# Kernel tuning notes

Measured on AMD Instinct MI355X. Metric: run time of the kernel, lower is better.

Reference implementation:

```python
import jax, jax.numpy as jnp
import numpy as np

N, E, IN, HID, H, C = 10000, 320000, 64, 64, 4, 64
HC = H * C  # 256


def setup_inputs() -> dict:
    key = jax.random.key(0)
    ks = jax.random.split(key, 40)
    ki = iter(range(40))
    def nrm(shape, scale=0.05):
        return jax.random.normal(ks[next(ki)], shape, dtype=jnp.float32) * scale
    inp = {
        "x": jax.random.normal(ks[next(ki)], (N, IN), dtype=jnp.float32),
        "edge_index": jax.random.randint(ks[next(ki)], (2, E), 0, N, dtype=jnp.int64),
        "lin_w": nrm((IN, HID)), "lin_b": nrm((HID,)),
    }
    dims_in = [HID, HC, HC]
    for i, di in enumerate(dims_in):
        inp[f"gat_w{i}"] = nrm((di, HC))
        inp[f"att_src{i}"] = nrm((H, C))
        inp[f"att_dst{i}"] = nrm((H, C))
        inp[f"gat_b{i}"] = nrm((HC,))
        inp[f"ln_g{i}"] = jnp.ones((HC,), jnp.float32)
        inp[f"ln_b{i}"] = jnp.zeros((HC,), jnp.float32)
    inp["ffn_w1"] = nrm((HC, 2 * HID)); inp["ffn_b1"] = nrm((2 * HID,))
    inp["ffn_w2"] = nrm((2 * HID, 64)); inp["ffn_b2"] = nrm((64,))
    return inp


def _layernorm(x, g, b, eps=1e-5):
    m = jnp.mean(x, -1, keepdims=True)
    v = jnp.var(x, -1, keepdims=True)
    return (x - m) * jax.lax.rsqrt(v + eps) * g + b


def _gat(x, src, dst, w, a_src, a_dst, b):
    # PyG GATConv: per-head linear, additive attention, segment softmax over dst
    xl = (x @ w).reshape(-1, H, C)              # [N,H,C]
    e = jax.nn.leaky_relu(jnp.sum(xl * a_src, -1)[src]
                          + jnp.sum(xl * a_dst, -1)[dst], 0.2)  # [E,H]
    emax = jax.ops.segment_max(e, dst, num_segments=N)
    ex = jnp.exp(e - emax[dst])
    alpha = ex / jax.ops.segment_sum(ex, dst, num_segments=N)[dst]
    out = jax.ops.segment_sum(xl[src] * alpha[:, :, None], dst, num_segments=N)
    return out.reshape(-1, HC) + b


def reference(x, edge_index, lin_w, lin_b,
              gat_w0, att_src0, att_dst0, gat_b0, ln_g0, ln_b0,
              gat_w1, att_src1, att_dst1, gat_b1, ln_g1, ln_b1,
              gat_w2, att_src2, att_dst2, gat_b2, ln_g2, ln_b2,
              ffn_w1, ffn_b1, ffn_w2, ffn_b2):
    loops = jnp.arange(N, dtype=edge_index.dtype)
    src = jnp.concatenate([edge_index[0], loops])  # add_self_loops=True
    dst = jnp.concatenate([edge_index[1], loops])
    h = jax.nn.relu(x @ lin_w + lin_b)
    layers = [(gat_w0, att_src0, att_dst0, gat_b0, ln_g0, ln_b0),
              (gat_w1, att_src1, att_dst1, gat_b1, ln_g1, ln_b1),
              (gat_w2, att_src2, att_dst2, gat_b2, ln_g2, ln_b2)]
    for (w, a_s, a_d, b, g, lb) in layers:
        residual = h
        h = jax.nn.elu(_gat(h, src, dst, w, a_s, a_d, b))
        if residual.shape[-1] != h.shape[-1]:
            residual = jnp.pad(residual, ((0, 0), (0, h.shape[-1] - residual.shape[-1])))
        h = _layernorm(h + residual, g, lb)  # dropout is identity in eval mode
    h = jax.nn.relu(h @ ffn_w1 + ffn_b1)
    return h @ ffn_w2 + ffn_b2
```

## Files before the change

### kernel.cpp

```cpp
#include <hip/hip_runtime.h>

#define N_NODES 10000
#define N_EDGES 320000
#define EL (N_EDGES + N_NODES)
#define HC 256
#define CAP 96

using bf16x8 = __attribute__((ext_vector_type(8))) short;
using f32x4  = __attribute__((ext_vector_type(4))) float;

__device__ __forceinline__ float bf2f(unsigned short u) {
  union { unsigned int i; float f; } v; v.i = ((unsigned int)u) << 16; return v.f;
}
__device__ __forceinline__ unsigned short f2bf(float f) {
  union { float f; unsigned int i; } v; v.f = f;
  unsigned int r = (v.i + 0x7FFFu + ((v.i >> 16) & 1u)) >> 16;
  return (unsigned short)r;
}


__device__ __forceinline__ void convw_body(const float* __restrict__ w,
                                           unsigned short* __restrict__ bt,
                                           int K, int idx) {
  int half = K >> 1;
  if (idx >= 256 * half) return;
  int col = idx / half;
  int k2 = (idx % half) * 2;
  ushort2 o;
  o.x = f2bf(w[(size_t)k2 * 256 + col]);
  o.y = f2bf(w[(size_t)(k2 + 1) * 256 + col]);
  *(ushort2*)(bt + (size_t)col * K + k2) = o;
}

__global__ __launch_bounds__(256) void prep_kernel(
    int* __restrict__ cnt,
    const float* __restrict__ w0, unsigned short* __restrict__ bt0,
    const float* __restrict__ w1, unsigned short* __restrict__ bt1,
    const float* __restrict__ w2, unsigned short* __restrict__ bt2) {
  int b = blockIdx.x, tid = threadIdx.x;
  if (b < 40) {
    int i = b * 256 + tid;
    if (i < N_NODES) cnt[i] = 0;
  } else if (b < 72) {
    convw_body(w0, bt0, 64, (b - 40) * 256 + tid);
  } else if (b < 200) {
    convw_body(w1, bt1, 256, (b - 72) * 256 + tid);
  } else {
    convw_body(w2, bt2, 256, (b - 200) * 256 + tid);
  }
}


__global__ __launch_bounds__(256) void scatter_lin_kernel(
    const int* __restrict__ edges, int* __restrict__ cnt, int* __restrict__ slots,
    const float* __restrict__ A, const float* __restrict__ B,
    const float* __restrict__ bias, float* __restrict__ C) {
  int tid = threadIdx.x;
  if (blockIdx.x < 1290) {
    int e = blockIdx.x * 256 + tid;
    if (e >= EL) return;
    int s, d;
    if (e < N_EDGES) { s = edges[e]; d = edges[N_EDGES + e]; }
    else { s = d = e - N_EDGES; }
    int pos = atomicAdd(&cnt[d], 1);
    slots[d * CAP + pos] = s;
    return;
  }
  __shared__ float As[16][36];
  __shared__ float Bs[32][64];
  int row0 = (blockIdx.x - 1290) * 16;
  int g = tid >> 6, lane = tid & 63;
  float acc[4];
#pragma unroll
  for (int r = 0; r < 4; ++r) acc[r] = 0.f;
  for (int k0 = 0; k0 < 64; k0 += 32) {
    if (tid < 128) {
      int r = tid >> 3;
      int kc = (tid & 7) << 2;
      *(float4*)&As[r][kc] = *(const float4*)(A + (size_t)(row0 + r) * 64 + k0 + kc);
    }
    {
      int idx = tid * 2;
#pragma unroll
      for (int i = 0; i < 2; ++i) {
        int fidx = (i * 256 + tid) * 4;
        int kk = fidx >> 6;
        int cc = fidx & 63;
        *(float4*)&Bs[kk][cc] = *(const float4*)(B + (size_t)(k0 + kk) * 64 + cc);
      }
      (void)idx;
    }
    __syncthreads();
#pragma unroll
    for (int kk = 0; kk < 32; kk += 4) {
      float a4[4][4];
#pragma unroll
      for (int rr = 0; rr < 4; ++rr) {
        float4 t = *(const float4*)&As[g * 4 + rr][kk];
        a4[rr][0] = t.x; a4[rr][1] = t.y; a4[rr][2] = t.z; a4[rr][3] = t.w;
      }
#pragma unroll
      for (int u = 0; u < 4; ++u) {
        float b = Bs[kk + u][lane];
#pragma unroll
        for (int rr = 0; rr < 4; ++rr) acc[rr] = fmaf(a4[rr][u], b, acc[rr]);
      }
    }
    __syncthreads();
  }
#pragma unroll
  for (int rr = 0; rr < 4; ++rr) {
    int row = row0 + g * 4 + rr;
    C[(size_t)row * 64 + lane] = fmaxf(acc[rr] + bias[lane], 0.f);
  }
}


template <int K>
__global__ __launch_bounds__(256) void gemm_attn_mfma(
    const float* __restrict__ A, const unsigned short* __restrict__ Bt,
    unsigned short* __restrict__ Cb,
    const float* __restrict__ att_src, const float* __restrict__ att_dst,
    float* __restrict__ asrc_out, float* __restrict__ adst_out) {
  __shared__ __align__(16) unsigned short Asw[16 * 64];
  __shared__ __align__(16) unsigned short Bsw[256 * 64];
  int tid = threadIdx.x;
  int wave = tid >> 6, lane = tid & 63;
  int r = lane & 15, g = lane >> 4;
  int row0 = blockIdx.x * 16;

  f32x4 acc[4];
#pragma unroll
  for (int i = 0; i < 4; ++i) acc[i] = {0.f, 0.f, 0.f, 0.f};

  for (int k0 = 0; k0 < K; k0 += 64) {
    {
      int ar = tid >> 4;
      int kc = (tid & 15) << 2;
      float4 av = *(const float4*)(A + (size_t)(row0 + ar) * K + k0 + kc);
      ushort4 o;
      o.x = f2bf(av.x); o.y = f2bf(av.y); o.z = f2bf(av.z); o.w = f2bf(av.w);
      *(ushort4*)((char*)Asw + ((ar * 128 + kc * 2) ^ ((ar & 7) << 4))) = o;
    }
#pragma unroll
    for (int i = 0; i < 8; ++i) {
      int idx = i * 256 + tid;
      int col = idx >> 3;
      int kc8 = idx & 7;
      uint4 v = *(const uint4*)(Bt + (size_t)col * K + k0 + kc8 * 8);
      *(uint4*)((char*)Bsw + ((col * 128 + kc8 * 16) ^ ((col & 7) << 4))) = v;
    }
    __syncthreads();
#pragma unroll
    for (int chunk = 0; chunk < 2; ++chunk) {
      bf16x8 af = *(const bf16x8*)((char*)Asw +
                    ((r * 128 + chunk * 64 + g * 16) ^ ((r & 7) << 4)));
#pragma unroll
      for (int i = 0; i < 4; ++i) {
        int col = (wave * 4 + i) * 16 + r;
        bf16x8 bfr = *(const bf16x8*)((char*)Bsw +
                       ((col * 128 + chunk * 64 + g * 16) ^ ((col & 7) << 4)));
        acc[i] = __builtin_amdgcn_mfma_f32_16x16x32_bf16(af, bfr, acc[i], 0, 0, 0);
      }
    }
    __syncthreads();
  }

  float asv[4], adv[4];
#pragma unroll
  for (int i = 0; i < 4; ++i) {
    int col = (wave * 4 + i) * 16 + r;
    asv[i] = att_src[col];
    adv[i] = att_dst[col];
  }
#pragma unroll
  for (int j = 0; j < 4; ++j) {
    float ps = acc[0][j] * asv[0] + acc[1][j] * asv[1] + acc[2][j] * asv[2] + acc[3][j] * asv[3];
    float pd = acc[0][j] * adv[0] + acc[1][j] * adv[1] + acc[2][j] * adv[2] + acc[3][j] * adv[3];
#pragma unroll
    for (int m = 8; m >= 1; m >>= 1) {
      ps += __shfl_xor(ps, m);
      pd += __shfl_xor(pd, m);
    }
    if (r == 0) {
      int row = row0 + g * 4 + j;
      asrc_out[row * 4 + wave] = ps;
      adst_out[row * 4 + wave] = pd;
    }
  }

#pragma unroll
  for (int i = 0; i < 4; ++i) {
    int col = (wave * 4 + i) * 16 + r;
#pragma unroll
    for (int j = 0; j < 4; ++j) {
      int row = row0 + g * 4 + j;
      Cb[(size_t)row * 256 + col] = f2bf(acc[i][j]);
    }
  }
}


template <int MODE>
__global__ __launch_bounds__(256) void agg_kernel(
    const int* __restrict__ cnt, const int* __restrict__ slots,
    const float* __restrict__ asrc, const float* __restrict__ adst,
    const unsigned short* __restrict__ xb, const float* __restrict__ bias,
    const float* __restrict__ resid, const float* __restrict__ ln_g,
    const float* __restrict__ ln_b, float* __restrict__ hout) {
  int w = threadIdx.x >> 6, lane = threadIdx.x & 63;
  int n = blockIdx.x * 4 + w;
  int h = lane >> 4;
  int ch = lane << 2;
  float ad = adst[n * 4 + h];

  int i0 = n * CAP, i1 = i0 + cnt[n];
  int last = i1 - 1;

  float4 acc = make_float4(0.f, 0.f, 0.f, 0.f);
  float wsum = 0.f;

  int sA[4];
#pragma unroll
  for (int j = 0; j < 4; ++j) sA[j] = slots[min(i0 + j, last)];
  float ca[4]; ushort4 cx[4];
#pragma unroll
  for (int j = 0; j < 4; ++j) {
    ca[j] = asrc[sA[j] * 4 + h];
    cx[j] = *(const ushort4*)(xb + (size_t)sA[j] * HC + ch);
  }
#pragma unroll
  for (int j = 0; j < 4; ++j) sA[j] = slots[min(i0 + 4 + j, last)];

#pragma unroll 2
  for (int base = i0; base < i1; base += 4) {
    float na[4]; ushort4 nx[4];
#pragma unroll
    for (int j = 0; j < 4; ++j) {
      na[j] = asrc[sA[j] * 4 + h];
      nx[j] = *(const ushort4*)(xb + (size_t)sA[j] * HC + ch);
    }
#pragma unroll
    for (int j = 0; j < 4; ++j) sA[j] = slots[min(base + 8 + j, last)];
#pragma unroll
    for (int j = 0; j < 4; ++j) {
      float e = ca[j] + ad;
      e = e > 0.f ? e : 0.2f * e;
      float wg = __expf(e);
      wg = (base + j < i1) ? wg : 0.f;
      wsum += wg;
      acc.x = fmaf(wg, bf2f(cx[j].x), acc.x);
      acc.y = fmaf(wg, bf2f(cx[j].y), acc.y);
      acc.z = fmaf(wg, bf2f(cx[j].z), acc.z);
      acc.w = fmaf(wg, bf2f(cx[j].w), acc.w);
    }
#pragma unroll
    for (int j = 0; j < 4; ++j) { ca[j] = na[j]; cx[j] = nx[j]; }
  }

  float rw = 1.f / wsum;
  float4 b4 = *(const float4*)(bias + ch);
  float v0 = fmaf(acc.x, rw, b4.x);
  float v1 = fmaf(acc.y, rw, b4.y);
  float v2 = fmaf(acc.z, rw, b4.z);
  float v3 = fmaf(acc.w, rw, b4.w);
  v0 = v0 > 0.f ? v0 : __expf(v0) - 1.f;
  v1 = v1 > 0.f ? v1 : __expf(v1) - 1.f;
  v2 = v2 > 0.f ? v2 : __expf(v2) - 1.f;
  v3 = v3 > 0.f ? v3 : __expf(v3) - 1.f;

  if constexpr (MODE == 0) {
    if (lane < 16) {
      float4 r = *(const float4*)(resid + (size_t)n * 64 + ch);
      v0 += r.x; v1 += r.y; v2 += r.z; v3 += r.w;
    }
  } else {
    float4 r = *(const float4*)(resid + (size_t)n * HC + ch);
    v0 += r.x; v1 += r.y; v2 += r.z; v3 += r.w;
  }

  float s1 = v0 + v1 + v2 + v3;
  float s2 = v0 * v0 + v1 * v1 + v2 * v2 + v3 * v3;
#pragma unroll
  for (int m = 32; m >= 1; m >>= 1) {
    s1 += __shfl_xor(s1, m);
    s2 += __shfl_xor(s2, m);
  }
  float mean = s1 * (1.f / 256.f);
  float var = s2 * (1.f / 256.f) - mean * mean;
  float inv = rsqrtf(var + 1e-5f);

  float4 g4 = *(const float4*)(ln_g + ch);
  float4 lb4 = *(const float4*)(ln_b + ch);
  float4 o;
  o.x = (v0 - mean) * inv * g4.x + lb4.x;
  o.y = (v1 - mean) * inv * g4.y + lb4.y;
  o.z = (v2 - mean) * inv * g4.z + lb4.z;
  o.w = (v3 - mean) * inv * g4.w + lb4.w;
  *(float4*)(hout + (size_t)n * HC + ch) = o;
}


__global__ __launch_bounds__(256) void ffn_kernel(const float* __restrict__ A,
                                                  const float* __restrict__ w1,
                                                  const float* __restrict__ b1,
                                                  const float* __restrict__ w2,
                                                  const float* __restrict__ b2,
                                                  float* __restrict__ out) {
  __shared__ float As[16][36];
  __shared__ float Bs[32][128];
  __shared__ float Ms[16][132];
  int tid = threadIdx.x;
  int row0 = blockIdx.x * 16;
  int g = tid >> 6, lane = tid & 63;

  {
    int colBase = lane * 2;
    float acc[4][2];
#pragma unroll
    for (int r = 0; r < 4; ++r) { acc[r][0] = 0.f; acc[r][1] = 0.f; }
    for (int k0 = 0; k0 < 256; k0 += 32) {
      if (tid < 128) {
        int r = tid >> 3;
        int kc = (tid & 7) << 2;
        *(float4*)&As[r][kc] = *(const float4*)(A + (size_t)(row0 + r) * 256 + k0 + kc);
      }
#pragma unroll
      for (int i = 0; i < 4; ++i) {
        int fidx = (i * 256 + tid) * 4;
        int kk = fidx >> 7;
        int cc = fidx & 127;
        *(float4*)&Bs[kk][cc] = *(const float4*)(w1 + (size_t)(k0 + kk) * 128 + cc);
      }
      __syncthreads();
#pragma unroll
      for (int kk = 0; kk < 32; kk += 4) {
        float a4[4][4];
#pragma unroll
        for (int rr = 0; rr < 4; ++rr) {
          float4 t = *(const float4*)&As[g * 4 + rr][kk];
          a4[rr][0] = t.x; a4[rr][1] = t.y; a4[rr][2] = t.z; a4[rr][3] = t.w;
        }
#pragma unroll
        for (int u = 0; u < 4; ++u) {
          float2 b = *(const float2*)&Bs[kk + u][colBase];
#pragma unroll
          for (int rr = 0; rr < 4; ++rr) {
            acc[rr][0] = fmaf(a4[rr][u], b.x, acc[rr][0]);
            acc[rr][1] = fmaf(a4[rr][u], b.y, acc[rr][1]);
          }
        }
      }
      __syncthreads();
    }
    float bb0 = b1[colBase], bb1 = b1[colBase + 1];
#pragma unroll
    for (int rr = 0; rr < 4; ++rr) {
      Ms[g * 4 + rr][colBase]     = fmaxf(acc[rr][0] + bb0, 0.f);
      Ms[g * 4 + rr][colBase + 1] = fmaxf(acc[rr][1] + bb1, 0.f);
    }
  }
  __syncthreads();

  {
    float acc[4];
#pragma unroll
    for (int r = 0; r < 4; ++r) acc[r] = 0.f;
    for (int k0 = 0; k0 < 128; k0 += 32) {
#pragma unroll
      for (int i = 0; i < 2; ++i) {
        int fidx = (i * 256 + tid) * 4;
        int kk = fidx >> 6;
        int cc = fidx & 63;
        *(float4*)&Bs[kk][cc] = *(const float4*)(w2 + (size_t)(k0 + kk) * 64 + cc);
      }
      __syncthreads();
#pragma unroll
      for (int kk = 0; kk < 32; ++kk) {
        float b = Bs[kk][lane];
#pragma unroll
        for (int rr = 0; rr < 4; ++rr)
          acc[rr] = fmaf(Ms[g * 4 + rr][k0 + kk], b, acc[rr]);
      }
      __syncthreads();
    }
    float bb = b2[lane];
#pragma unroll
    for (int rr = 0; rr < 4; ++rr) {
      int row = row0 + g * 4 + rr;
      out[(size_t)row * 64 + lane] = acc[rr] + bb;
    }
  }
}


extern "C" void kernel_launch(void* const* d_in, const int* in_sizes, int n_in,
                              void* d_out, int out_size, void* d_ws, size_t ws_size,
                              hipStream_t stream) {
  (void)in_sizes; (void)n_in; (void)out_size; (void)ws_size;
  const float* x      = (const float*)d_in[0];
  const int*   edges  = (const int*)d_in[1];
  const float* lin_w  = (const float*)d_in[2];
  const float* lin_b  = (const float*)d_in[3];
  const float* gat_w[3] = {(const float*)d_in[4], (const float*)d_in[10], (const float*)d_in[16]};
  const float* att_s[3] = {(const float*)d_in[5], (const float*)d_in[11], (const float*)d_in[17]};
  const float* att_d[3] = {(const float*)d_in[6], (const float*)d_in[12], (const float*)d_in[18]};
  const float* gat_b[3] = {(const float*)d_in[7], (const float*)d_in[13], (const float*)d_in[19]};
  const float* ln_g[3]  = {(const float*)d_in[8], (const float*)d_in[14], (const float*)d_in[20]};
  const float* ln_b[3]  = {(const float*)d_in[9], (const float*)d_in[15], (const float*)d_in[21]};
  const float* ffn_w1 = (const float*)d_in[22];
  const float* ffn_b1 = (const float*)d_in[23];
  const float* ffn_w2 = (const float*)d_in[24];
  const float* ffn_b2 = (const float*)d_in[25];

  char* p = (char*)d_ws;
  auto alloc = [&](size_t bytes) {
    char* q = p;
    p += (bytes + 255) & ~(size_t)255;
    return q;
  };
  int* cnt   = (int*)alloc(N_NODES * 4);
  int* slots = (int*)alloc((size_t)N_NODES * CAP * 4);
  float* h0  = (float*)alloc((size_t)N_NODES * 64 * 4);
  float* hA  = (float*)alloc((size_t)N_NODES * HC * 4);
  float* hB  = (float*)alloc((size_t)N_NODES * HC * 4);
  unsigned short* xb = (unsigned short*)alloc((size_t)N_NODES * HC * 2);
  float* as4 = (float*)alloc((size_t)N_NODES * 16);
  float* ad4 = (float*)alloc((size_t)N_NODES * 16);
  unsigned short* bt0 = (unsigned short*)alloc(256 * 64 * 2);
  unsigned short* bt1 = (unsigned short*)alloc(256 * 256 * 2);
  unsigned short* bt2 = (unsigned short*)alloc(256 * 256 * 2);

  const int gblk = N_NODES / 16;
  const int nblk = N_NODES / 4;

  prep_kernel<<<328, 256, 0, stream>>>(cnt, gat_w[0], bt0, gat_w[1], bt1, gat_w[2], bt2);
  scatter_lin_kernel<<<1290 + 625, 256, 0, stream>>>(edges, cnt, slots, x, lin_w, lin_b, h0);

  gemm_attn_mfma<64><<<gblk, 256, 0, stream>>>(h0, bt0, xb, att_s[0], att_d[0], as4, ad4);
  agg_kernel<0><<<nblk, 256, 0, stream>>>(cnt, slots, as4, ad4, xb, gat_b[0], h0,
                                          ln_g[0], ln_b[0], hA);
  gemm_attn_mfma<256><<<gblk, 256, 0, stream>>>(hA, bt1, xb, att_s[1], att_d[1], as4, ad4);
  agg_kernel<1><<<nblk, 256, 0, stream>>>(cnt, slots, as4, ad4, xb, gat_b[1], hA,
                                          ln_g[1], ln_b[1], hB);
  gemm_attn_mfma<256><<<gblk, 256, 0, stream>>>(hB, bt2, xb, att_s[2], att_d[2], as4, ad4);
  agg_kernel<1><<<nblk, 256, 0, stream>>>(cnt, slots, as4, ad4, xb, gat_b[2], hB,
                                          ln_g[2], ln_b[2], hA);

  ffn_kernel<<<gblk, 256, 0, stream>>>(hA, ffn_w1, ffn_b1, ffn_w2, ffn_b2, (float*)d_out);
}
```

Baseline: 165.5 us.

## Split each node's edge list across wave halves with 16-byte feature gathers

The aggregation kernel now has each wave's two 32-lane halves process disjoint halves of a node's neighbor list, and each lane loads 8 bf16 channels (16 bytes) per neighbor instead of 4. Partial sums and weight totals are combined with a cross-half shuffle, and each lane then handles 4 output channels for bias, ELU, residual and layernorm. This halves the serial per-node edge loop and uses wider gather loads, at the cost of more registers, an extra reduction step, and dropping the explicit unroll pragma.

```diff
diff --git a/kernel.cpp b/kernel.cpp
--- a/kernel.cpp
+++ b/kernel.cpp
@@ -80,7 +80,6 @@
       *(float4*)&As[r][kc] = *(const float4*)(A + (size_t)(row0 + r) * 64 + k0 + kc);
     }
     {
-      int idx = tid * 2;
 #pragma unroll
       for (int i = 0; i < 2; ++i) {
         int fidx = (i * 256 + tid) * 4;
@@ -88,7 +87,6 @@
         int cc = fidx & 63;
         *(float4*)&Bs[kk][cc] = *(const float4*)(B + (size_t)(k0 + kk) * 64 + cc);
       }
-      (void)idx;
     }
     __syncthreads();
 #pragma unroll
@@ -210,35 +208,40 @@
     const float* __restrict__ ln_b, float* __restrict__ hout) {
   int w = threadIdx.x >> 6, lane = threadIdx.x & 63;
   int n = blockIdx.x * 4 + w;
-  int h = lane >> 4;
-  int ch = lane << 2;
+  int lh = lane & 31;
+  int half = lane >> 5;
+  int h = lh >> 3;
+  int ch8 = lh << 3;
   float ad = adst[n * 4 + h];
 
-  int i0 = n * CAP, i1 = i0 + cnt[n];
-  int last = i1 - 1;
-
-  float4 acc = make_float4(0.f, 0.f, 0.f, 0.f);
+  int i0 = n * CAP;
+  int deg = cnt[n];
+  int len0 = (deg + 1) >> 1;
+  int beg = i0 + (half ? len0 : 0);
+  int end = i0 + (half ? deg : len0);
+  int last = end - 1;
+
+  float a0 = 0.f, a1 = 0.f, a2 = 0.f, a3 = 0.f, a4 = 0.f, a5 = 0.f, a6 = 0.f, a7 = 0.f;
   float wsum = 0.f;
 
   int sA[4];
 #pragma unroll
-  for (int j = 0; j < 4; ++j) sA[j] = slots[min(i0 + j, last)];
-  float ca[4]; ushort4 cx[4];
+  for (int j = 0; j < 4; ++j) sA[j] = slots[min(beg + j, last)];
+  float ca[4]; uint4 cx[4];
 #pragma unroll
   for (int j = 0; j < 4; ++j) {
     ca[j] = asrc[sA[j] * 4 + h];
-    cx[j] = *(const ushort4*)(xb + (size_t)sA[j] * HC + ch);
-  }
-#pragma unroll
-  for (int j = 0; j < 4; ++j) sA[j] = slots[min(i0 + 4 + j, last)];
-
-#pragma unroll 2
-  for (int base = i0; base < i1; base += 4) {
-    float na[4]; ushort4 nx[4];
+    cx[j] = *(const uint4*)(xb + (size_t)sA[j] * HC + ch8);
+  }
+#pragma unroll
+  for (int j = 0; j < 4; ++j) sA[j] = slots[min(beg + 4 + j, last)];
+
+  for (int base = beg; base < end; base += 4) {
+    float na[4]; uint4 nx[4];
 #pragma unroll
     for (int j = 0; j < 4; ++j) {
       na[j] = asrc[sA[j] * 4 + h];
-      nx[j] = *(const ushort4*)(xb + (size_t)sA[j] * HC + ch);
+      nx[j] = *(const uint4*)(xb + (size_t)sA[j] * HC + ch8);
     }
 #pragma unroll
     for (int j = 0; j < 4; ++j) sA[j] = slots[min(base + 8 + j, last)];
@@ -247,35 +250,51 @@
       float e = ca[j] + ad;
       e = e > 0.f ? e : 0.2f * e;
       float wg = __expf(e);
-      wg = (base + j < i1) ? wg : 0.f;
+      wg = (base + j < end) ? wg : 0.f;
       wsum += wg;
-      acc.x = fmaf(wg, bf2f(cx[j].x), acc.x);
-      acc.y = fmaf(wg, bf2f(cx[j].y), acc.y);
-      acc.z = fmaf(wg, bf2f(cx[j].z), acc.z);
-      acc.w = fmaf(wg, bf2f(cx[j].w), acc.w);
+      a0 = fmaf(wg, bf2f((unsigned short)(cx[j].x & 0xffff)), a0);
+      a1 = fmaf(wg, bf2f((unsigned short)(cx[j].x >> 16)), a1);
+      a2 = fmaf(wg, bf2f((unsigned short)(cx[j].y & 0xffff)), a2);
+      a3 = fmaf(wg, bf2f((unsigned short)(cx[j].y >> 16)), a3);
+      a4 = fmaf(wg, bf2f((unsigned short)(cx[j].z & 0xffff)), a4);
+      a5 = fmaf(wg, bf2f((unsigned short)(cx[j].z >> 16)), a5);
+      a6 = fmaf(wg, bf2f((unsigned short)(cx[j].w & 0xffff)), a6);
+      a7 = fmaf(wg, bf2f((unsigned short)(cx[j].w >> 16)), a7);
     }
 #pragma unroll
     for (int j = 0; j < 4; ++j) { ca[j] = na[j]; cx[j] = nx[j]; }
   }
 
+  a0 += __shfl_xor(a0, 32); a1 += __shfl_xor(a1, 32);
+  a2 += __shfl_xor(a2, 32); a3 += __shfl_xor(a3, 32);
+  a4 += __shfl_xor(a4, 32); a5 += __shfl_xor(a5, 32);
+  a6 += __shfl_xor(a6, 32); a7 += __shfl_xor(a7, 32);
+  wsum += __shfl_xor(wsum, 32);
+
+  int cb = ch8 + half * 4;
+  float v0 = half ? a4 : a0;
+  float v1 = half ? a5 : a1;
+  float v2 = half ? a6 : a2;
+  float v3 = half ? a7 : a3;
+
   float rw = 1.f / wsum;
-  float4 b4 = *(const float4*)(bias + ch);
-  float v0 = fmaf(acc.x, rw, b4.x);
-  float v1 = fmaf(acc.y, rw, b4.y);
-  float v2 = fmaf(acc.z, rw, b4.z);
-  float v3 = fmaf(acc.w, rw, b4.w);
+  float4 b4 = *(const float4*)(bias + cb);
+  v0 = fmaf(v0, rw, b4.x);
+  v1 = fmaf(v1, rw, b4.y);
+  v2 = fmaf(v2, rw, b4.z);
+  v3 = fmaf(v3, rw, b4.w);
   v0 = v0 > 0.f ? v0 : __expf(v0) - 1.f;
   v1 = v1 > 0.f ? v1 : __expf(v1) - 1.f;
   v2 = v2 > 0.f ? v2 : __expf(v2) - 1.f;
   v3 = v3 > 0.f ? v3 : __expf(v3) - 1.f;
 
   if constexpr (MODE == 0) {
-    if (lane < 16) {
-      float4 r = *(const float4*)(resid + (size_t)n * 64 + ch);
+    if (cb < 64) {
+      float4 r = *(const float4*)(resid + (size_t)n * 64 + cb);
       v0 += r.x; v1 += r.y; v2 += r.z; v3 += r.w;
     }
   } else {
-    float4 r = *(const float4*)(resid + (size_t)n * HC + ch);
+    float4 r = *(const float4*)(resid + (size_t)n * HC + cb);
     v0 += r.x; v1 += r.y; v2 += r.z; v3 += r.w;
   }
 
@@ -290,14 +309,14 @@
   float var = s2 * (1.f / 256.f) - mean * mean;
   float inv = rsqrtf(var + 1e-5f);
 
-  float4 g4 = *(const float4*)(ln_g + ch);
-  float4 lb4 = *(const float4*)(ln_b + ch);
+  float4 g4 = *(const float4*)(ln_g + cb);
+  float4 lb4 = *(const float4*)(ln_b + cb);
   float4 o;
   o.x = (v0 - mean) * inv * g4.x + lb4.x;
   o.y = (v1 - mean) * inv * g4.y + lb4.y;
   o.z = (v2 - mean) * inv * g4.z + lb4.z;
   o.w = (v3 - mean) * inv * g4.w + lb4.w;
-  *(float4*)(hout + (size_t)n * HC + ch) = o;
+  *(float4*)(hout + (size_t)n * HC + cb) = o;
 }
 
 
```

New measurement: 153.9 us. -7.0%, faster.
